# Performance work log

Hardware: AMD Instinct MI355X
Metric: run time of the kernel (lower is better)

Reference implementation:

```python
import jax, jax.numpy as jnp
import numpy as np

WS = 7          # window size (square)
SHIFT = 3       # shift size
NH = 8          # num heads
DIM = 256
B, H, W = 32, 56, 56


def _relative_position_index(ws: int) -> np.ndarray:
    coords = np.stack(np.meshgrid(np.arange(ws), np.arange(ws), indexing='ij'))  # (2, ws, ws)
    cf = coords.reshape(2, -1)                                                   # (2, N)
    rel = cf[:, :, None] - cf[:, None, :]                                        # (2, N, N)
    rel = rel.transpose(1, 2, 0).copy()
    rel[:, :, 0] += ws - 1
    rel[:, :, 1] += ws - 1
    rel[:, :, 0] *= 2 * ws - 1
    return rel.sum(-1).reshape(-1).astype(np.int32)                              # (N*N,)


def _shift_mask(h: int, w: int, ws: int, shift: int) -> np.ndarray:
    img = np.zeros((h, w), dtype=np.float32)
    cnt = 0
    for hs in ((0, -ws), (-ws, -shift), (-shift, None)):
        for wsl in ((0, -ws), (-ws, -shift), (-shift, None)):
            img[hs[0]:hs[1], wsl[0]:wsl[1]] = cnt
            cnt += 1
    nwh, nww = h // ws, w // ws
    m = img.reshape(nwh, ws, nww, ws).transpose(0, 2, 1, 3).reshape(nwh * nww, ws * ws)
    am = m[:, None, :] - m[:, :, None]                 # (nW, N, N)
    return np.where(am != 0, np.float32(-100.0), np.float32(0.0))


def setup_inputs() -> dict:
    key = jax.random.key(0)
    ks = jax.random.split(key, 5)
    x = jax.random.normal(ks[0], (B, H, W, DIM), jnp.float32)
    qkv_weight = jax.random.normal(ks[1], (3 * DIM, DIM), jnp.float32) * 0.02
    qkv_bias = jnp.zeros((3 * DIM,), jnp.float32)
    proj_weight = jax.random.normal(ks[2], (DIM, DIM), jnp.float32) * 0.02
    proj_bias = jnp.zeros((DIM,), jnp.float32)
    rel_bias_table = jax.random.normal(ks[3], ((2 * WS - 1) ** 2, NH), jnp.float32) * 0.02
    rel_pos_index = jnp.asarray(_relative_position_index(WS))
    return {
        'x': x, 'qkv_weight': qkv_weight, 'qkv_bias': qkv_bias,
        'proj_weight': proj_weight, 'proj_bias': proj_bias,
        'rel_bias_table': rel_bias_table, 'rel_pos_index': rel_pos_index,
    }


def reference(x, qkv_weight, qkv_bias, proj_weight, proj_bias, rel_bias_table, rel_pos_index):
    b, h, w, c = x.shape
    n = WS * WS
    hd = c // NH
    nwh, nww = h // WS, w // WS
    nw = nwh * nww

    # relative position bias: (1, NH, N, N)
    bias = rel_bias_table[rel_pos_index].reshape(n, n, NH).transpose(2, 0, 1)[None]

    # cyclic shift
    xs = jnp.roll(x, (-SHIFT, -SHIFT), axis=(1, 2))

    # window partition -> (B*nW, N, C)
    xw = xs.reshape(b, nwh, WS, nww, WS, c).transpose(0, 1, 3, 2, 4, 5).reshape(b * nw, n, c)

    qkv = xw @ qkv_weight.T + qkv_bias
    qkv = qkv.reshape(b * nw, n, 3, NH, hd).transpose(2, 0, 3, 1, 4)  # (3, B*nW, NH, N, hd)
    q = qkv[0] * (hd ** -0.5)
    k = qkv[1]
    v = qkv[2]

    attn = jnp.einsum('bhnd,bhmd->bhnm', q, k) + bias                # (B*nW, NH, N, N)

    # shift mask (static)
    amask = jnp.asarray(_shift_mask(h, w, WS, SHIFT))                # (nW, N, N)
    attn = attn.reshape(b, nw, NH, n, n) + amask[None, :, None]
    attn = jax.nn.softmax(attn.reshape(b * nw, NH, n, n), axis=-1)

    out = jnp.einsum('bhnm,bhmd->bhnd', attn, v)                     # (B*nW, NH, N, hd)
    out = out.transpose(0, 2, 1, 3).reshape(b * nw, n, c)
    out = out @ proj_weight.T + proj_bias

    # window reverse + reverse shift
    out = out.reshape(b, nwh, nww, WS, WS, c).transpose(0, 1, 3, 2, 4, 5).reshape(b, h, w, c)
    out = jnp.roll(out, (SHIFT, SHIFT), axis=(1, 2))
    return out
```

## Files before the change

kernel.cpp:

```cpp
#include <hip/hip_runtime.h>
#include <hip/hip_bf16.h>


#define NTOK 49
#define DIM_ 256
#define NH_  8
#define NQKV 196608
#define NPRJ 65536
#define NTAB1 19208
#define NTAB4 (4 * NTAB1)

#define WSP_B  393216ull
#define TAB_B  524288ull
#define Q_B    831744ull
#define QK_EL  25690112
#define Q_BYTES 51380224ull
#define K_B    (Q_B + Q_BYTES)
#define VT_B   (K_B + Q_BYTES)
#define VT_BYTES 58720256ull
#define NEED_BIG (VT_B + VT_BYTES)
#define NEED_TAB (TAB_B + (unsigned long long)NTAB4 * 4)

typedef short v8s __attribute__((ext_vector_type(8)));
typedef float v4f __attribute__((ext_vector_type(4)));
typedef float v16f __attribute__((ext_vector_type(16)));

#define MFMA16 __builtin_amdgcn_mfma_f32_16x16x32_bf16
#define MFMA32 __builtin_amdgcn_mfma_f32_32x32x16_bf16
#define LGKM_WAIT() asm volatile("s_waitcnt lgkmcnt(0)" ::: "memory")

static __device__ __forceinline__ v8s zero_v8s() {
    v8s z = {0, 0, 0, 0, 0, 0, 0, 0};
    return z;
}

static __device__ __forceinline__ v16f zero_v16f() {
    v16f z;
    #pragma unroll
    for (int i = 0; i < 16; ++i) z[i] = 0.0f;
    return z;
}

static __device__ __forceinline__ v8s lds_frag(const __hip_bfloat16* p, int row,
                                               int stride, int koff, int nrows) {
    if (row < nrows) return *(const v8s*)(p + row * stride + koff);
    return zero_v8s();
}

static __device__ __forceinline__ v8s cvt8(const float* p) {
    v4f a = *(const v4f*)p;
    v4f b = *(const v4f*)(p + 4);
    union { v8s v; __hip_bfloat16 h[8]; } r;
    r.h[0] = __float2bfloat16(a[0]); r.h[1] = __float2bfloat16(a[1]);
    r.h[2] = __float2bfloat16(a[2]); r.h[3] = __float2bfloat16(a[3]);
    r.h[4] = __float2bfloat16(b[0]); r.h[5] = __float2bfloat16(b[1]);
    r.h[6] = __float2bfloat16(b[2]); r.h[7] = __float2bfloat16(b[3]);
    return r.v;
}

__global__ __launch_bounds__(256) void prep_kernel(
    const float* __restrict__ qkvW, const float* __restrict__ projW,
    const float* __restrict__ rbt, const int* __restrict__ rpi,
    __hip_bfloat16* __restrict__ wsQ, __hip_bfloat16* __restrict__ wsP,
    float* __restrict__ tab4, int doTab)
{
    int i = blockIdx.x * 256 + threadIdx.x;
    if (i < NQKV) { wsQ[i] = __float2bfloat16(qkvW[i]); return; }
    int j = i - NQKV;
    if (j < NPRJ) { wsP[j] = __float2bfloat16(projW[j]); return; }
    int t = j - NPRJ;
    if (!doTab || t >= NTAB4) return;
    int cls = t / NTAB1, rem = t - cls * NTAB1;
    int h = rem / 2401, p = rem - h * 2401;
    int row = p / 49, col = p - row * 49;
    int rh = (cls & 1) ? (((row / 7) < 4) ? 1 : 2) : 0;
    int rw = (cls & 2) ? (((row % 7) < 4) ? 1 : 2) : 0;
    int ch = (cls & 1) ? (((col / 7) < 4) ? 1 : 2) : 0;
    int cw = (cls & 2) ? (((col % 7) < 4) ? 1 : 2) : 0;
    float mask = ((rh * 3 + rw) != (ch * 3 + cw)) ? -100.0f : 0.0f;
    tab4[t] = rbt[rpi[p] * NH_ + h] + mask;
}

__global__ __launch_bounds__(256, 4) void qkv_kernel(
    const float* __restrict__ x,
    const float* __restrict__ qkvB,
    const __hip_bfloat16* __restrict__ wsQ,
    __hip_bfloat16* __restrict__ Q,
    __hip_bfloat16* __restrict__ K,
    __hip_bfloat16* __restrict__ VT)
{
    constexpr int SXS = 264;
    __shared__ alignas(16) __hip_bfloat16 s_x[NTOK * SXS];

    const int tid = threadIdx.x, wave = tid >> 6, lane = tid & 63;
    const int l32 = lane & 31, half = lane >> 5;
    const int win = blockIdx.x;
    const int b = win >> 6, wh = (win >> 3) & 7, wwi = win & 7;

    for (int i = tid; i < NTOK * 64; i += 256) {
        int tok = i >> 6, f4 = (i & 63) * 4;
        int r = tok / 7, c = tok - r * 7;
        int hg = wh * 7 + r + 3; if (hg >= 56) hg -= 56;
        int wg = wwi * 7 + c + 3; if (wg >= 56) wg -= 56;
        float4 v = *(const float4*)(x + ((b * 56 + hg) * 56 + wg) * DIM_ + f4);
        __hip_bfloat16* dst = s_x + tok * SXS + f4;
        dst[0] = __float2bfloat16(v.x);
        dst[1] = __float2bfloat16(v.y);
        dst[2] = __float2bfloat16(v.z);
        dst[3] = __float2bfloat16(v.w);
    }
    for (int i = tid; i < 256 * 7; i += 256) {
        int fg = i / 7, col = 49 + (i - fg * 7);
        int h = fg >> 5, feat = fg & 31;
        VT[((win * NH_ + h) * 32 + feat) * 56 + col] = __float2bfloat16(0.0f);
    }
    __syncthreads();

    const float qscale = 0.17677669529663687f;
    const int r1 = (32 + l32 < NTOK) ? (32 + l32) : 0;

    for (int t = 0; t < 6; ++t) {
        const int nb = (wave * 6 + t) * 32;
        const int mat = nb >> 8;
        const int h = (nb >> 5) & 7;
        const __hip_bfloat16* wrow  = wsQ + (nb + l32) * DIM_ + half * 8;
        const __hip_bfloat16* arow0 = s_x + l32 * SXS + half * 8;
        const __hip_bfloat16* arow1 = s_x + r1 * SXS + half * 8;

        v16f acc0 = zero_v16f(), acc1 = zero_v16f();

        if (mat < 2) {
            #pragma unroll
            for (int kh = 0; kh < 2; ++kh) {
                v8s wf[8];
                #pragma unroll
                for (int k = 0; k < 8; ++k)
                    wf[k] = *(const v8s*)(wrow + kh * 128 + k * 16);
                #pragma unroll
                for (int k = 0; k < 8; ++k) {
                    v8s a0 = *(const v8s*)(arow0 + kh * 128 + k * 16);
                    v8s a1 = *(const v8s*)(arow1 + kh * 128 + k * 16);
                    acc0 = MFMA32(a0, wf[k], acc0, 0, 0, 0);
                    acc1 = MFMA32(a1, wf[k], acc1, 0, 0, 0);
                }
            }
            float bias = qkvB[nb + l32];
            float sc = (mat == 0) ? qscale : 1.0f;
            __hip_bfloat16* dst = (mat == 0 ? Q : K) + (win * NH_ + h) * (NTOK * 32) + l32;
            #pragma unroll
            for (int rg = 0; rg < 16; ++rg) {
                int rowoff = (rg & 3) + 8 * (rg >> 2) + 4 * half;
                dst[rowoff * 32] = __float2bfloat16((acc0[rg] + bias) * sc);
                int tok1 = 32 + rowoff;
                if (tok1 < NTOK)
                    dst[tok1 * 32] = __float2bfloat16((acc1[rg] + bias) * sc);
            }
        } else {
            #pragma unroll
            for (int kh = 0; kh < 2; ++kh) {
                v8s wf[8];
                #pragma unroll
                for (int k = 0; k < 8; ++k)
                    wf[k] = *(const v8s*)(wrow + kh * 128 + k * 16);
                #pragma unroll
                for (int k = 0; k < 8; ++k) {
                    v8s b0 = *(const v8s*)(arow0 + kh * 128 + k * 16);
                    v8s b1 = *(const v8s*)(arow1 + kh * 128 + k * 16);
                    acc0 = MFMA32(wf[k], b0, acc0, 0, 0, 0);
                    acc1 = MFMA32(wf[k], b1, acc1, 0, 0, 0);
                }
            }
            __hip_bfloat16* dst = VT + (win * NH_ + h) * (32 * 56);
            const int tok1 = 32 + l32;
            #pragma unroll
            for (int rg = 0; rg < 16; ++rg) {
                int feat = (rg & 3) + 8 * (rg >> 2) + 4 * half;
                float bias = qkvB[nb + feat];
                dst[feat * 56 + l32] = __float2bfloat16(acc0[rg] + bias);
                if (tok1 < NTOK)
                    dst[feat * 56 + tok1] = __float2bfloat16(acc1[rg] + bias);
            }
        }
    }
}

__global__ __launch_bounds__(256) void attn_kernel(
    const float* __restrict__ tab4,
    const __hip_bfloat16* __restrict__ K,
    const __hip_bfloat16* __restrict__ VT,
    __hip_bfloat16* __restrict__ Q)
{
    constexpr int PS = 72;
    __shared__ alignas(16) __hip_bfloat16 s_p[4][NTOK * PS];

    const int tid = threadIdx.x, wave = tid >> 6, lane = tid & 63;
    const int quad = lane >> 4, l16 = lane & 15;
    const int id = blockIdx.x * 4 + wave;
    const int win = id >> 3, h = id & 7;
    const int wh = (win >> 3) & 7, wwi = win & 7;
    const int cls = ((wh == 7) ? 1 : 0) | ((wwi == 7) ? 2 : 0);
    const float* tabh = tab4 + (cls * NH_ + h) * 2401;
    __hip_bfloat16* qs = Q + (win * NH_ + h) * (NTOK * 32);
    const __hip_bfloat16* ks_ = K + (win * NH_ + h) * (NTOK * 32);
    const __hip_bfloat16* vts = VT + (win * NH_ + h) * (32 * 56);
    __hip_bfloat16* wp = s_p[wave];

    v8s qa[4], kb[4];
    #pragma unroll
    for (int mt = 0; mt < 4; ++mt) {
        int tok = mt * 16 + l16;
        qa[mt] = *(const v8s*)(qs + tok * 32 + quad * 8);
        kb[mt] = *(const v8s*)(ks_ + tok * 32 + quad * 8);
    }
    v8s pb[2][2];
    #pragma unroll
    for (int nt = 0; nt < 2; ++nt) {
        const __hip_bfloat16* vr = vts + (nt * 16 + l16) * 56;
        pb[nt][0] = *(const v8s*)(vr + quad * 8);
        pb[nt][1] = (quad == 3) ? zero_v8s() : *(const v8s*)(vr + 32 + quad * 8);
    }

    #pragma unroll
    for (int mtile = 0; mtile < 4; ++mtile) {
        v4f sa[4];
        #pragma unroll
        for (int nt = 0; nt < 4; ++nt) {
            v4f z = {0.f, 0.f, 0.f, 0.f};
            sa[nt] = MFMA16(qa[mtile], kb[nt], z, 0, 0, 0);
        }
        #pragma unroll
        for (int rg = 0; rg < 4; ++rg) {
            int row = mtile * 16 + quad * 4 + rg;
            bool rok = row < NTOK;
            float v[4];
            float rmax = -1e30f;
            #pragma unroll
            for (int nt = 0; nt < 4; ++nt) {
                int col = nt * 16 + l16;
                float s = -1e30f;
                if (rok && col < NTOK)
                    s = sa[nt][rg] + tabh[row * 49 + col];
                v[nt] = s;
                rmax = fmaxf(rmax, s);
            }
            #pragma unroll
            for (int mm = 8; mm >= 1; mm >>= 1)
                rmax = fmaxf(rmax, __shfl_xor(rmax, mm, 64));
            float rsum = 0.f;
            #pragma unroll
            for (int nt = 0; nt < 4; ++nt) {
                float e = (v[nt] <= -1e29f) ? 0.f : __expf(v[nt] - rmax);
                v[nt] = e;
                rsum += e;
            }
            #pragma unroll
            for (int mm = 8; mm >= 1; mm >>= 1)
                rsum += __shfl_xor(rsum, mm, 64);
            if (rok) {
                float inv = 1.0f / rsum;
                #pragma unroll
                for (int nt = 0; nt < 4; ++nt)
                    wp[row * PS + nt * 16 + l16] = __float2bfloat16(v[nt] * inv);
            }
        }
    }
    LGKM_WAIT();

    #pragma unroll
    for (int mtile = 0; mtile < 4; ++mtile) {
        v8s pa0 = lds_frag(wp, mtile * 16 + l16, PS, quad * 8, NTOK);
        v8s pa1 = lds_frag(wp, mtile * 16 + l16, PS, 32 + quad * 8, NTOK);
        #pragma unroll
        for (int nt = 0; nt < 2; ++nt) {
            v4f z = {0.f, 0.f, 0.f, 0.f};
            v4f acc = MFMA16(pa0, pb[nt][0], z, 0, 0, 0);
            acc = MFMA16(pa1, pb[nt][1], acc, 0, 0, 0);
            #pragma unroll
            for (int rg = 0; rg < 4; ++rg) {
                int tok = mtile * 16 + quad * 4 + rg;
                if (tok < NTOK)
                    qs[tok * 32 + nt * 16 + l16] = __float2bfloat16(acc[rg]);
            }
        }
    }
}

__global__ __launch_bounds__(256) void proj_kernel(
    const __hip_bfloat16* __restrict__ OH,
    const __hip_bfloat16* __restrict__ wsP,
    const float* __restrict__ projB,
    float* __restrict__ out)
{
    const int tid = threadIdx.x, wave = tid >> 6, lane = tid & 63;
    const int quad = lane >> 4, l16 = lane & 15;
    const int win = blockIdx.x;
    const int b = win >> 6, wh = (win >> 3) & 7, wwi = win & 7;
    const int m0 = wave * 16;

    const __hip_bfloat16* ohw = OH + (size_t)win * (NH_ * NTOK * 32);
    v8s af[8];
    int tokA = m0 + l16;
    #pragma unroll
    for (int ks = 0; ks < 8; ++ks)
        af[ks] = (tokA < NTOK)
                   ? *(const v8s*)(ohw + ks * (NTOK * 32) + tokA * 32 + quad * 8)
                   : zero_v8s();

    int ooff[4];
    #pragma unroll
    for (int rg = 0; rg < 4; ++rg) {
        int row = m0 + quad * 4 + rg;
        if (row < NTOK) {
            int r = row / 7, c = row - r * 7;
            int hg = wh * 7 + r + 3; if (hg >= 56) hg -= 56;
            int wg = wwi * 7 + c + 3; if (wg >= 56) wg -= 56;
            ooff[rg] = ((b * 56 + hg) * 56 + wg) * DIM_;
        } else ooff[rg] = -1;
    }

    #pragma unroll
    for (int t = 0; t < 16; ++t) {
        const __hip_bfloat16* wrow = wsP + (t * 16 + l16) * DIM_;
        v4f acc = {0.f, 0.f, 0.f, 0.f};
        #pragma unroll
        for (int ks = 0; ks < 8; ++ks) {
            v8s bfr = *(const v8s*)(wrow + ks * 32 + quad * 8);
            acc = MFMA16(af[ks], bfr, acc, 0, 0, 0);
        }
        float pbv = projB[t * 16 + l16];
        #pragma unroll
        for (int rg = 0; rg < 4; ++rg)
            if (ooff[rg] >= 0)
                out[ooff[rg] + t * 16 + l16] = acc[rg] + pbv;
    }
}

__global__ __launch_bounds__(256, 2) void swin_attn_fused(
    const float* __restrict__ x,
    const float* __restrict__ qkvB,
    const float* __restrict__ projB,
    const float* __restrict__ rbt,
    const int*   __restrict__ rpi,
    const __hip_bfloat16* __restrict__ wsQ,
    const __hip_bfloat16* __restrict__ wsP,
    const float* __restrict__ biasTab,
    float*       __restrict__ out)
{
    constexpr int QKS = 40;
    constexpr int VTS = 72;
    constexpr int PS  = 72;
    constexpr int OS  = 264;
    constexpr int WVSZ = 6224;

    __shared__ alignas(16) __hip_bfloat16 s_wv[4 * WVSZ];
    __shared__ alignas(16) __hip_bfloat16 s_o[NTOK * OS];
    __shared__ int s_off[NTOK];
    __shared__ int s_reg[NTOK];

    const int tid  = threadIdx.x;
    const int wave = tid >> 6;
    const int lane = tid & 63;
    const int quad = lane >> 4;
    const int l16  = lane & 15;

    const int wid  = blockIdx.x;
    const int b    = wid >> 6;
    const int wIdx = wid & 63;
    const int wh   = wIdx >> 3;
    const int wwi  = wIdx & 7;

    if (tid < NTOK) {
        int r = tid / 7, c = tid - r * 7;
        int hs = wh * 7 + r, ws = wwi * 7 + c;
        int hg = hs + 3; if (hg >= 56) hg -= 56;
        int wg = ws + 3; if (wg >= 56) wg -= 56;
        s_off[tid] = ((b * 56 + hg) * 56 + wg) * DIM_;
        int rh = (hs < 49) ? 0 : ((hs < 53) ? 1 : 2);
        int rw = (ws < 49) ? 0 : ((ws < 53) ? 1 : 2);
        s_reg[tid] = rh * 3 + rw;
    }

    __hip_bfloat16* wq  = s_wv + wave * WVSZ;
    __hip_bfloat16* wk  = wq + NTOK * QKS;
    __hip_bfloat16* wvt = wq + 2 * NTOK * QKS;
    __hip_bfloat16* wp  = wq;

    for (int i = lane; i < 32 * 15; i += 64) {
        int f = i / 15, kk = 49 + (i % 15);
        wvt[f * VTS + kk] = __float2bfloat16(0.0f);
    }
    __syncthreads();

    const float qscale = 0.17677669529663687f;

    for (int hp = 0; hp < 2; ++hp) {
        const int h = wave * 2 + hp;
        LGKM_WAIT();

        for (int mh = 0; mh < 2; ++mh) {
            const int mbase = mh * 32;
            v8s at[2][8];
            #pragma unroll
            for (int sub = 0; sub < 2; ++sub) {
                int tok = mbase + sub * 16 + l16;
                const float* xr = (tok < NTOK) ? (x + s_off[tok]) : nullptr;
                #pragma unroll
                for (int ks = 0; ks < 8; ++ks)
                    at[sub][ks] = xr ? cvt8(xr + ks * 32 + quad * 8) : zero_v8s();
            }
            #pragma unroll
            for (int t = 0; t < 6; ++t) {
                int mat = t >> 1, ntile = t & 1;
                int nout = mat * 256 + h * 32 + ntile * 16 + l16;
                const __hip_bfloat16* wrow = wsQ + nout * DIM_;
                v4f a0 = {0.f, 0.f, 0.f, 0.f}, a1 = {0.f, 0.f, 0.f, 0.f};
                #pragma unroll
                for (int ks = 0; ks < 8; ++ks) {
                    v8s bfr = *(const v8s*)(wrow + ks * 32 + quad * 8);
                    a0 = MFMA16(at[0][ks], bfr, a0, 0, 0, 0);
                    a1 = MFMA16(at[1][ks], bfr, a1, 0, 0, 0);
                }
                float bias  = qkvB[nout];
                float scale = (mat == 0) ? qscale : 1.0f;
                #pragma unroll
                for (int sub = 0; sub < 2; ++sub) {
                    v4f acc = sub ? a1 : a0;
                    #pragma unroll
                    for (int rg = 0; rg < 4; ++rg) {
                        int row = mbase + sub * 16 + quad * 4 + rg;
                        if (row < NTOK) {
                            float val = (acc[rg] + bias) * scale;
                            int col = ntile * 16 + l16;
                            __hip_bfloat16 bv = __float2bfloat16(val);
                            if (mat == 0)      wq[row * QKS + col] = bv;
                            else if (mat == 1) wk[row * QKS + col] = bv;
                            else               wvt[col * VTS + row] = bv;
                        }
                    }
                }
            }
        }
        LGKM_WAIT();

        v8s qa[4], kb[4];
        #pragma unroll
        for (int i = 0; i < 4; ++i) {
            qa[i] = lds_frag(wq, i * 16 + l16, QKS, quad * 8, NTOK);
            kb[i] = lds_frag(wk, i * 16 + l16, QKS, quad * 8, NTOK);
        }
        int regc[4];
        #pragma unroll
        for (int nt = 0; nt < 4; ++nt) {
            int col = nt * 16 + l16;
            regc[nt] = (col < NTOK) ? s_reg[col] : -1;
        }
        LGKM_WAIT();
        const float* tabh = biasTab ? (biasTab + h * 2401) : nullptr;
        #pragma unroll
        for (int mtile = 0; mtile < 4; ++mtile) {
            v4f sa[4];
            #pragma unroll
            for (int nt = 0; nt < 4; ++nt) {
                v4f z = {0.f, 0.f, 0.f, 0.f};
                sa[nt] = MFMA16(qa[mtile], kb[nt], z, 0, 0, 0);
            }
            #pragma unroll
            for (int rg = 0; rg < 4; ++rg) {
                int row = mtile * 16 + quad * 4 + rg;
                bool rok = row < NTOK;
                int rr = rok ? s_reg[row] : -2;
                float v[4];
                float rmax = -1e30f;
                #pragma unroll
                for (int nt = 0; nt < 4; ++nt) {
                    int col = nt * 16 + l16;
                    float s = -1e30f;
                    if (rok && col < NTOK) {
                        float bv = tabh ? tabh[row * 49 + col]
                                        : rbt[rpi[row * 49 + col] * NH_ + h];
                        s = sa[nt][rg] + bv;
                        if (rr != regc[nt]) s -= 100.0f;
                    }
                    v[nt] = s;
                    rmax = fmaxf(rmax, s);
                }
                #pragma unroll
                for (int mm = 8; mm >= 1; mm >>= 1)
                    rmax = fmaxf(rmax, __shfl_xor(rmax, mm, 64));
                float rsum = 0.f;
                #pragma unroll
                for (int nt = 0; nt < 4; ++nt) {
                    float e = (v[nt] <= -1e29f) ? 0.f : __expf(v[nt] - rmax);
                    v[nt] = e;
                    rsum += e;
                }
                #pragma unroll
                for (int mm = 8; mm >= 1; mm >>= 1)
                    rsum += __shfl_xor(rsum, mm, 64);
                if (rok) {
                    float inv = 1.0f / rsum;
                    #pragma unroll
                    for (int nt = 0; nt < 4; ++nt)
                        wp[row * PS + nt * 16 + l16] = __float2bfloat16(v[nt] * inv);
                }
            }
        }
        LGKM_WAIT();

        v8s pb[2][2];
        #pragma unroll
        for (int nt = 0; nt < 2; ++nt)
            #pragma unroll
            for (int ks = 0; ks < 2; ++ks)
                pb[nt][ks] = *(const v8s*)(wvt + (nt * 16 + l16) * VTS + ks * 32 + quad * 8);
        #pragma unroll
        for (int mtile = 0; mtile < 4; ++mtile) {
            v8s pa0 = lds_frag(wp, mtile * 16 + l16, PS, quad * 8, NTOK);
            v8s pa1 = lds_frag(wp, mtile * 16 + l16, PS, 32 + quad * 8, NTOK);
            #pragma unroll
            for (int nt = 0; nt < 2; ++nt) {
                v4f z = {0.f, 0.f, 0.f, 0.f};
                v4f acc = MFMA16(pa0, pb[nt][0], z, 0, 0, 0);
                acc = MFMA16(pa1, pb[nt][1], acc, 0, 0, 0);
                #pragma unroll
                for (int rg = 0; rg < 4; ++rg) {
                    int row = mtile * 16 + quad * 4 + rg;
                    if (row < NTOK)
                        s_o[row * OS + h * 32 + nt * 16 + l16] = __float2bfloat16(acc[rg]);
                }
            }
        }
    }
    __syncthreads();

    {
        int m0 = wave * 16;
        v8s af[8];
        #pragma unroll
        for (int ks = 0; ks < 8; ++ks)
            af[ks] = lds_frag(s_o, m0 + l16, OS, ks * 32 + quad * 8, NTOK);
        #pragma unroll
        for (int t = 0; t < 16; ++t) {
            const __hip_bfloat16* wrow = wsP + (t * 16 + l16) * DIM_;
            v4f acc = {0.f, 0.f, 0.f, 0.f};
            #pragma unroll
            for (int ks = 0; ks < 8; ++ks) {
                v8s bfr = *(const v8s*)(wrow + ks * 32 + quad * 8);
                acc = MFMA16(af[ks], bfr, acc, 0, 0, 0);
            }
            float pbv = projB[t * 16 + l16];
            #pragma unroll
            for (int rg = 0; rg < 4; ++rg) {
                int row = m0 + quad * 4 + rg;
                if (row < NTOK)
                    out[s_off[row] + t * 16 + l16] = acc[rg] + pbv;
            }
        }
    }
}

extern "C" void kernel_launch(void* const* d_in, const int* in_sizes, int n_in,
                              void* d_out, int out_size, void* d_ws, size_t ws_size,
                              hipStream_t stream) {
    const float* x     = (const float*)d_in[0];
    const float* qkvW  = (const float*)d_in[1];
    const float* qkvB  = (const float*)d_in[2];
    const float* projW = (const float*)d_in[3];
    const float* projB = (const float*)d_in[4];
    const float* rbt   = (const float*)d_in[5];
    const int*   rpi   = (const int*)d_in[6];
    float* o = (float*)d_out;

    __hip_bfloat16* wsQ = (__hip_bfloat16*)d_ws;
    __hip_bfloat16* wsP = (__hip_bfloat16*)((char*)d_ws + WSP_B);
    float* tab4         = (float*)((char*)d_ws + TAB_B);
    __hip_bfloat16* Q   = (__hip_bfloat16*)((char*)d_ws + Q_B);
    __hip_bfloat16* K   = (__hip_bfloat16*)((char*)d_ws + K_B);
    __hip_bfloat16* VT  = (__hip_bfloat16*)((char*)d_ws + VT_B);

    const int prepBlocks = (NQKV + NPRJ + NTAB4 + 255) / 256;

    if (ws_size >= NEED_BIG) {
        prep_kernel<<<prepBlocks, 256, 0, stream>>>(qkvW, projW, rbt, rpi,
                                                    wsQ, wsP, tab4, 1);
        qkv_kernel<<<2048, 256, 0, stream>>>(x, qkvB, wsQ, Q, K, VT);
        attn_kernel<<<4096, 256, 0, stream>>>(tab4, K, VT, Q);
        proj_kernel<<<2048, 256, 0, stream>>>(Q, wsP, projB, o);
    } else {
        int doTab = (ws_size >= NEED_TAB) ? 1 : 0;
        prep_kernel<<<prepBlocks, 256, 0, stream>>>(qkvW, projW, rbt, rpi,
                                                    wsQ, wsP, tab4, doTab);
        swin_attn_fused<<<2048, 256, 0, stream>>>(x, qkvB, projB, rbt, rpi,
                                                  wsQ, wsP, doTab ? tab4 : nullptr, o);
    }
}
```

Baseline: 503.5 us.

## Fuse QKV projection and window attention into one kernel via per-wave LDS

```diff
diff --git a/kernel.cpp b/kernel.cpp
--- a/kernel.cpp
+++ b/kernel.cpp
@@ -13,7 +13,6 @@
 #define WSP_B  393216ull
 #define TAB_B  524288ull
 #define Q_B    831744ull
-#define QK_EL  25690112
 #define Q_BYTES 51380224ull
 #define K_B    (Q_B + Q_BYTES)
 #define VT_B   (K_B + Q_BYTES)
@@ -81,21 +80,36 @@
     tab4[t] = rbt[rpi[p] * NH_ + h] + mask;
 }
 
-__global__ __launch_bounds__(256, 4) void qkv_kernel(
+__global__ __launch_bounds__(256) void qkvattn_kernel(
     const float* __restrict__ x,
     const float* __restrict__ qkvB,
     const __hip_bfloat16* __restrict__ wsQ,
-    __hip_bfloat16* __restrict__ Q,
-    __hip_bfloat16* __restrict__ K,
-    __hip_bfloat16* __restrict__ VT)
+    const float* __restrict__ tab4,
+    __hip_bfloat16* __restrict__ OH)
 {
     constexpr int SXS = 264;
+    constexpr int QKS = 40;
+    constexpr int VTS = 72;
+    constexpr int PS  = 72;
+    constexpr int WVSZ = 2 * NTOK * QKS + 32 * VTS;
+
     __shared__ alignas(16) __hip_bfloat16 s_x[NTOK * SXS];
+    __shared__ alignas(16) __hip_bfloat16 s_wv[4 * WVSZ];
 
     const int tid = threadIdx.x, wave = tid >> 6, lane = tid & 63;
+    const int quad = lane >> 4, l16 = lane & 15;
     const int l32 = lane & 31, half = lane >> 5;
     const int win = blockIdx.x;
     const int b = win >> 6, wh = (win >> 3) & 7, wwi = win & 7;
+    const int cls = ((wh == 7) ? 1 : 0) | ((wwi == 7) ? 2 : 0);
+
+    __hip_bfloat16* wq  = s_wv + wave * WVSZ;
+    __hip_bfloat16* wk  = wq + NTOK * QKS;
+    __hip_bfloat16* wvt = wq + 2 * NTOK * QKS;
+    __hip_bfloat16* wp  = wq;
+
+    for (int i = lane; i < 32 * 7; i += 64)
+        wvt[(i / 7) * VTS + 49 + (i % 7)] = __float2bfloat16(0.0f);
 
     for (int i = tid; i < NTOK * 64; i += 256) {
         int tok = i >> 6, f4 = (i & 63) * 4;
@@ -109,179 +123,160 @@
         dst[2] = __float2bfloat16(v.z);
         dst[3] = __float2bfloat16(v.w);
     }
-    for (int i = tid; i < 256 * 7; i += 256) {
-        int fg = i / 7, col = 49 + (i - fg * 7);
-        int h = fg >> 5, feat = fg & 31;
-        VT[((win * NH_ + h) * 32 + feat) * 56 + col] = __float2bfloat16(0.0f);
-    }
     __syncthreads();
 
     const float qscale = 0.17677669529663687f;
     const int r1 = (32 + l32 < NTOK) ? (32 + l32) : 0;
-
-    for (int t = 0; t < 6; ++t) {
-        const int nb = (wave * 6 + t) * 32;
-        const int mat = nb >> 8;
-        const int h = (nb >> 5) & 7;
-        const __hip_bfloat16* wrow  = wsQ + (nb + l32) * DIM_ + half * 8;
-        const __hip_bfloat16* arow0 = s_x + l32 * SXS + half * 8;
-        const __hip_bfloat16* arow1 = s_x + r1 * SXS + half * 8;
-
-        v16f acc0 = zero_v16f(), acc1 = zero_v16f();
-
-        if (mat < 2) {
-            #pragma unroll
-            for (int kh = 0; kh < 2; ++kh) {
-                v8s wf[8];
-                #pragma unroll
-                for (int k = 0; k < 8; ++k)
-                    wf[k] = *(const v8s*)(wrow + kh * 128 + k * 16);
-                #pragma unroll
-                for (int k = 0; k < 8; ++k) {
-                    v8s a0 = *(const v8s*)(arow0 + kh * 128 + k * 16);
-                    v8s a1 = *(const v8s*)(arow1 + kh * 128 + k * 16);
-                    acc0 = MFMA32(a0, wf[k], acc0, 0, 0, 0);
-                    acc1 = MFMA32(a1, wf[k], acc1, 0, 0, 0);
-                }
-            }
-            float bias = qkvB[nb + l32];
-            float sc = (mat == 0) ? qscale : 1.0f;
-            __hip_bfloat16* dst = (mat == 0 ? Q : K) + (win * NH_ + h) * (NTOK * 32) + l32;
-            #pragma unroll
-            for (int rg = 0; rg < 16; ++rg) {
-                int rowoff = (rg & 3) + 8 * (rg >> 2) + 4 * half;
-                dst[rowoff * 32] = __float2bfloat16((acc0[rg] + bias) * sc);
-                int tok1 = 32 + rowoff;
-                if (tok1 < NTOK)
-                    dst[tok1 * 32] = __float2bfloat16((acc1[rg] + bias) * sc);
-            }
-        } else {
-            #pragma unroll
-            for (int kh = 0; kh < 2; ++kh) {
-                v8s wf[8];
-                #pragma unroll
-                for (int k = 0; k < 8; ++k)
-                    wf[k] = *(const v8s*)(wrow + kh * 128 + k * 16);
-                #pragma unroll
-                for (int k = 0; k < 8; ++k) {
-                    v8s b0 = *(const v8s*)(arow0 + kh * 128 + k * 16);
-                    v8s b1 = *(const v8s*)(arow1 + kh * 128 + k * 16);
-                    acc0 = MFMA32(wf[k], b0, acc0, 0, 0, 0);
-                    acc1 = MFMA32(wf[k], b1, acc1, 0, 0, 0);
-                }
-            }
-            __hip_bfloat16* dst = VT + (win * NH_ + h) * (32 * 56);
-            const int tok1 = 32 + l32;
-            #pragma unroll
-            for (int rg = 0; rg < 16; ++rg) {
-                int feat = (rg & 3) + 8 * (rg >> 2) + 4 * half;
-                float bias = qkvB[nb + feat];
-                dst[feat * 56 + l32] = __float2bfloat16(acc0[rg] + bias);
-                if (tok1 < NTOK)
-                    dst[feat * 56 + tok1] = __float2bfloat16(acc1[rg] + bias);
-            }
-        }
-    }
-}
-
-__global__ __launch_bounds__(256) void attn_kernel(
-    const float* __restrict__ tab4,
-    const __hip_bfloat16* __restrict__ K,
-    const __hip_bfloat16* __restrict__ VT,
-    __hip_bfloat16* __restrict__ Q)
-{
-    constexpr int PS = 72;
-    __shared__ alignas(16) __hip_bfloat16 s_p[4][NTOK * PS];
-
-    const int tid = threadIdx.x, wave = tid >> 6, lane = tid & 63;
-    const int quad = lane >> 4, l16 = lane & 15;
-    const int id = blockIdx.x * 4 + wave;
-    const int win = id >> 3, h = id & 7;
-    const int wh = (win >> 3) & 7, wwi = win & 7;
-    const int cls = ((wh == 7) ? 1 : 0) | ((wwi == 7) ? 2 : 0);
-    const float* tabh = tab4 + (cls * NH_ + h) * 2401;
-    __hip_bfloat16* qs = Q + (win * NH_ + h) * (NTOK * 32);
-    const __hip_bfloat16* ks_ = K + (win * NH_ + h) * (NTOK * 32);
-    const __hip_bfloat16* vts = VT + (win * NH_ + h) * (32 * 56);
-    __hip_bfloat16* wp = s_p[wave];
-
-    v8s qa[4], kb[4];
-    #pragma unroll
-    for (int mt = 0; mt < 4; ++mt) {
-        int tok = mt * 16 + l16;
-        qa[mt] = *(const v8s*)(qs + tok * 32 + quad * 8);
-        kb[mt] = *(const v8s*)(ks_ + tok * 32 + quad * 8);
-    }
-    v8s pb[2][2];
-    #pragma unroll
-    for (int nt = 0; nt < 2; ++nt) {
-        const __hip_bfloat16* vr = vts + (nt * 16 + l16) * 56;
-        pb[nt][0] = *(const v8s*)(vr + quad * 8);
-        pb[nt][1] = (quad == 3) ? zero_v8s() : *(const v8s*)(vr + 32 + quad * 8);
-    }
-
-    #pragma unroll
-    for (int mtile = 0; mtile < 4; ++mtile) {
-        v4f sa[4];
-        #pragma unroll
-        for (int nt = 0; nt < 4; ++nt) {
-            v4f z = {0.f, 0.f, 0.f, 0.f};
-            sa[nt] = MFMA16(qa[mtile], kb[nt], z, 0, 0, 0);
-        }
-        #pragma unroll
-        for (int rg = 0; rg < 4; ++rg) {
-            int row = mtile * 16 + quad * 4 + rg;
-            bool rok = row < NTOK;
-            float v[4];
-            float rmax = -1e30f;
+    const __hip_bfloat16* arow0 = s_x + l32 * SXS + half * 8;
+    const __hip_bfloat16* arow1 = s_x + r1 * SXS + half * 8;
+
+    for (int hp = 0; hp < 2; ++hp) {
+        const int h = wave * 2 + hp;
+
+        #pragma unroll
+        for (int m = 0; m < 3; ++m) {
+            const int nb = m * 256 + h * 32;
+            const __hip_bfloat16* wrow = wsQ + (nb + l32) * DIM_ + half * 8;
+            v16f acc0 = zero_v16f(), acc1 = zero_v16f();
+
+            if (m < 2) {
+                #pragma unroll
+                for (int kh = 0; kh < 2; ++kh) {
+                    v8s wf[8];
+                    #pragma unroll
+                    for (int k = 0; k < 8; ++k)
+                        wf[k] = *(const v8s*)(wrow + kh * 128 + k * 16);
+                    #pragma unroll
+                    for (int k = 0; k < 8; ++k) {
+                        v8s a0 = *(const v8s*)(arow0 + kh * 128 + k * 16);
+                        v8s a1 = *(const v8s*)(arow1 + kh * 128 + k * 16);
+                        acc0 = MFMA32(a0, wf[k], acc0, 0, 0, 0);
+                        acc1 = MFMA32(a1, wf[k], acc1, 0, 0, 0);
+                    }
+                }
+                float bias = qkvB[nb + l32];
+                float sc = (m == 0) ? qscale : 1.0f;
+                __hip_bfloat16* dst = (m == 0) ? wq : wk;
+                #pragma unroll
+                for (int rg = 0; rg < 16; ++rg) {
+                    int rowoff = (rg & 3) + 8 * (rg >> 2) + 4 * half;
+                    dst[rowoff * QKS + l32] =
+                        __float2bfloat16((acc0[rg] + bias) * sc);
+                    int tok1 = 32 + rowoff;
+                    if (tok1 < NTOK)
+                        dst[tok1 * QKS + l32] =
+                            __float2bfloat16((acc1[rg] + bias) * sc);
+                }
+            } else {
+                #pragma unroll
+                for (int kh = 0; kh < 2; ++kh) {
+                    v8s wf[8];
+                    #pragma unroll
+                    for (int k = 0; k < 8; ++k)
+                        wf[k] = *(const v8s*)(wrow + kh * 128 + k * 16);
+                    #pragma unroll
+                    for (int k = 0; k < 8; ++k) {
+                        v8s b0 = *(const v8s*)(arow0 + kh * 128 + k * 16);
+                        v8s b1 = *(const v8s*)(arow1 + kh * 128 + k * 16);
+                        acc0 = MFMA32(wf[k], b0, acc0, 0, 0, 0);
+                        acc1 = MFMA32(wf[k], b1, acc1, 0, 0, 0);
+                    }
+                }
+                const int tok1 = 32 + l32;
+                #pragma unroll
+                for (int rg = 0; rg < 16; ++rg) {
+                    int feat = (rg & 3) + 8 * (rg >> 2) + 4 * half;
+                    float bias = qkvB[nb + feat];
+                    wvt[feat * VTS + l32] = __float2bfloat16(acc0[rg] + bias);
+                    if (tok1 < NTOK)
+                        wvt[feat * VTS + tok1] = __float2bfloat16(acc1[rg] + bias);
+                }
+            }
+        }
+        LGKM_WAIT();
+
+        const float* tabh = tab4 + (cls * NH_ + h) * 2401;
+        __hip_bfloat16* qs = OH + (win * NH_ + h) * (NTOK * 32);
+
+        v8s qa[4], kb[4];
+        #pragma unroll
+        for (int mt = 0; mt < 4; ++mt) {
+            qa[mt] = lds_frag(wq, mt * 16 + l16, QKS, quad * 8, NTOK);
+            kb[mt] = lds_frag(wk, mt * 16 + l16, QKS, quad * 8, NTOK);
+        }
+        v8s pb[2][2];
+        #pragma unroll
+        for (int nt = 0; nt < 2; ++nt) {
+            const __hip_bfloat16* vr = wvt + (nt * 16 + l16) * VTS;
+            pb[nt][0] = *(const v8s*)(vr + quad * 8);
+            pb[nt][1] = (quad == 3) ? zero_v8s() : *(const v8s*)(vr + 32 + quad * 8);
+        }
+        LGKM_WAIT();
+
+        #pragma unroll
+        for (int mtile = 0; mtile < 4; ++mtile) {
+            v4f sa[4];
             #pragma unroll
             for (int nt = 0; nt < 4; ++nt) {
-                int col = nt * 16 + l16;
-                float s = -1e30f;
-                if (rok && col < NTOK)
-                    s = sa[nt][rg] + tabh[row * 49 + col];
-                v[nt] = s;
-                rmax = fmaxf(rmax, s);
-            }
-            #pragma unroll
-            for (int mm = 8; mm >= 1; mm >>= 1)
-                rmax = fmaxf(rmax, __shfl_xor(rmax, mm, 64));
-            float rsum = 0.f;
-            #pragma unroll
-            for (int nt = 0; nt < 4; ++nt) {
-                float e = (v[nt] <= -1e29f) ? 0.f : __expf(v[nt] - rmax);
-                v[nt] = e;
-                rsum += e;
-            }
-            #pragma unroll
-            for (int mm = 8; mm >= 1; mm >>= 1)
-                rsum += __shfl_xor(rsum, mm, 64);
-            if (rok) {
-                float inv = 1.0f / rsum;
-                #pragma unroll
-                for (int nt = 0; nt < 4; ++nt)
-                    wp[row * PS + nt * 16 + l16] = __float2bfloat16(v[nt] * inv);
-            }
-        }
-    }
-    LGKM_WAIT();
-
-    #pragma unroll
-    for (int mtile = 0; mtile < 4; ++mtile) {
-        v8s pa0 = lds_frag(wp, mtile * 16 + l16, PS, quad * 8, NTOK);
-        v8s pa1 = lds_frag(wp, mtile * 16 + l16, PS, 32 + quad * 8, NTOK);
-        #pragma unroll
-        for (int nt = 0; nt < 2; ++nt) {
-            v4f z = {0.f, 0.f, 0.f, 0.f};
-            v4f acc = MFMA16(pa0, pb[nt][0], z, 0, 0, 0);
-            acc = MFMA16(pa1, pb[nt][1], acc, 0, 0, 0);
+                v4f z = {0.f, 0.f, 0.f, 0.f};
+                sa[nt] = MFMA16(qa[mtile], kb[nt], z, 0, 0, 0);
+            }
             #pragma unroll
             for (int rg = 0; rg < 4; ++rg) {
-                int tok = mtile * 16 + quad * 4 + rg;
-                if (tok < NTOK)
-                    qs[tok * 32 + nt * 16 + l16] = __float2bfloat16(acc[rg]);
-            }
-        }
+                int row = mtile * 16 + quad * 4 + rg;
+                bool rok = row < NTOK;
+                float v[4];
+                float rmax = -1e30f;
+                #pragma unroll
+                for (int nt = 0; nt < 4; ++nt) {
+                    int col = nt * 16 + l16;
+                    float s = -1e30f;
+                    if (rok && col < NTOK)
+                        s = sa[nt][rg] + tabh[row * 49 + col];
+                    v[nt] = s;
+                    rmax = fmaxf(rmax, s);
+                }
+                #pragma unroll
+                for (int mm = 8; mm >= 1; mm >>= 1)
+                    rmax = fmaxf(rmax, __shfl_xor(rmax, mm, 64));
+                float rsum = 0.f;
+                #pragma unroll
+                for (int nt = 0; nt < 4; ++nt) {
+                    float e = (v[nt] <= -1e29f) ? 0.f : __expf(v[nt] - rmax);
+                    v[nt] = e;
+                    rsum += e;
+                }
+                #pragma unroll
+                for (int mm = 8; mm >= 1; mm >>= 1)
+                    rsum += __shfl_xor(rsum, mm, 64);
+                if (rok) {
+                    float inv = 1.0f / rsum;
+                    #pragma unroll
+                    for (int nt = 0; nt < 4; ++nt)
+                        wp[row * PS + nt * 16 + l16] = __float2bfloat16(v[nt] * inv);
+                }
+            }
+        }
+        LGKM_WAIT();
+
+        #pragma unroll
+        for (int mtile = 0; mtile < 4; ++mtile) {
+            v8s pa0 = lds_frag(wp, mtile * 16 + l16, PS, quad * 8, NTOK);
+            v8s pa1 = lds_frag(wp, mtile * 16 + l16, PS, 32 + quad * 8, NTOK);
+            #pragma unroll
+            for (int nt = 0; nt < 2; ++nt) {
+                v4f z = {0.f, 0.f, 0.f, 0.f};
+                v4f acc = MFMA16(pa0, pb[nt][0], z, 0, 0, 0);
+                acc = MFMA16(pa1, pb[nt][1], acc, 0, 0, 0);
+                #pragma unroll
+                for (int rg = 0; rg < 4; ++rg) {
+                    int tok = mtile * 16 + quad * 4 + rg;
+                    if (tok < NTOK)
+                        qs[tok * 32 + nt * 16 + l16] = __float2bfloat16(acc[rg]);
+                }
+            }
+        }
+        LGKM_WAIT();
     }
 }
 
@@ -574,18 +569,15 @@
     __hip_bfloat16* wsQ = (__hip_bfloat16*)d_ws;
     __hip_bfloat16* wsP = (__hip_bfloat16*)((char*)d_ws + WSP_B);
     float* tab4         = (float*)((char*)d_ws + TAB_B);
-    __hip_bfloat16* Q   = (__hip_bfloat16*)((char*)d_ws + Q_B);
-    __hip_bfloat16* K   = (__hip_bfloat16*)((char*)d_ws + K_B);
-    __hip_bfloat16* VT  = (__hip_bfloat16*)((char*)d_ws + VT_B);
+    __hip_bfloat16* OH  = (__hip_bfloat16*)((char*)d_ws + Q_B);
 
     const int prepBlocks = (NQKV + NPRJ + NTAB4 + 255) / 256;
 
     if (ws_size >= NEED_BIG) {
         prep_kernel<<<prepBlocks, 256, 0, stream>>>(qkvW, projW, rbt, rpi,
                                                     wsQ, wsP, tab4, 1);
-        qkv_kernel<<<2048, 256, 0, stream>>>(x, qkvB, wsQ, Q, K, VT);
-        attn_kernel<<<4096, 256, 0, stream>>>(tab4, K, VT, Q);
-        proj_kernel<<<2048, 256, 0, stream>>>(Q, wsP, projB, o);
+        qkvattn_kernel<<<2048, 256, 0, stream>>>(x, qkvB, wsQ, tab4, OH);
+        proj_kernel<<<2048, 256, 0, stream>>>(OH, wsP, projB, o);
     } else {
         int doTab = (ws_size >= NEED_TAB) ? 1 : 0;
         prep_kernel<<<prepBlocks, 256, 0, stream>>>(qkvW, projW, rbt, rpi,
```

Result: faster. 486.6 us (-3.4%).
